# Kernel tuning notes

Measured on AMD Instinct MI355X. Metric: run time of the kernel, lower is better.

Reference implementation:

```python
import jax, jax.numpy as jnp
import numpy as np

BETA = 0.25
EPS = 1e-10


def setup_inputs() -> dict:
    key = jax.random.key(0)
    k1, k2 = jax.random.split(key)
    z = jax.random.normal(k1, (16, 256, 32, 32), dtype=jnp.float32)
    # Original init: uniform(-1/n_embed, 1/n_embed)
    n_embed, embed_dim = 8192, 256
    codebook = jax.random.uniform(k2, (n_embed, embed_dim), dtype=jnp.float32,
                                  minval=-1.0 / n_embed, maxval=1.0 / n_embed)
    return {"z": z, "codebook": codebook}


def reference(z, codebook):
    B, C, H, W = z.shape
    n_embed = codebook.shape[0]
    zp = jnp.transpose(z, (0, 2, 3, 1))            # (B,H,W,C)
    zf = zp.reshape(-1, C)                          # (N,C)
    # squared L2 distances (N, n_embed)
    d = (jnp.sum(zf * zf, axis=1, keepdims=True)
         + jnp.sum(codebook * codebook, axis=1)
         - 2.0 * zf @ codebook.T)
    idx = jnp.argmin(d, axis=1)                     # (N,)
    zq = codebook[idx].reshape(zp.shape)            # gather == one-hot @ codebook
    commitment_loss = jnp.mean((jax.lax.stop_gradient(zq) - zp) ** 2)
    embedding_loss = jnp.mean((zq - jax.lax.stop_gradient(zp)) ** 2)
    loss = embedding_loss + BETA * commitment_loss
    # straight-through estimator
    zq_st = zp + jax.lax.stop_gradient(zq - zp)
    # perplexity from mean one-hot usage (counts / N)
    counts = jnp.zeros((n_embed,), dtype=zf.dtype).at[idx].add(1.0)
    avg_probs = counts / zf.shape[0]
    perplexity = jnp.exp(-jnp.sum(avg_probs * jnp.log(avg_probs + EPS)))
    zq_out = jnp.transpose(zq_st, (0, 3, 1, 2))     # (B,C,H,W)
    return zq_out, loss, perplexity, idx
```

## Files before the change

kernel.cpp:

```cpp
#include <hip/hip_runtime.h>
#include <math.h>

#define Nrows 16384
#define NE 8192
#define Kdim 256
#define HWsz 1024
#define NSPL 4
#define BETAF 0.25f

typedef __attribute__((ext_vector_type(8))) short bf16x8;
typedef __attribute__((ext_vector_type(16))) float f32x16;
typedef unsigned short u16;

__device__ inline u16 bf16_rne(float x) {
  unsigned int u = __float_as_uint(x);
  return (u16)((u + 0x7FFFu + ((u >> 16) & 1u)) >> 16);
}
__device__ inline float bf16_tof(u16 h) {
  return __uint_as_float(((unsigned int)h) << 16);
}
__device__ inline void gll16(const void* g, void* l) {
  __builtin_amdgcn_global_load_lds(
      (const __attribute__((address_space(1))) unsigned int*)g,
      (__attribute__((address_space(3))) unsigned int*)l, 16, 0, 0);
}

__global__ __launch_bounds__(256) void cc_kernel(const float* __restrict__ cb,
                                                 float* __restrict__ cc) {
  int wave = threadIdx.x >> 6;
  int lane = threadIdx.x & 63;
  int row = blockIdx.x * 4 + wave;
  const float4 v = *(const float4*)(cb + (size_t)row * Kdim + lane * 4);
  float s = v.x * v.x + v.y * v.y + v.z * v.z + v.w * v.w;
  for (int off = 32; off; off >>= 1) s += __shfl_down(s, off);
  if (lane == 0) cc[row] = s;
}

__global__ __launch_bounds__(256) void conv_cb(const float* __restrict__ cb,
                                               u16* __restrict__ Cf) {
  const int g = blockIdx.x * 256 + threadIdx.x;
  const int j = g >> 4, k16 = g & 15;
  const float* src = cb + (size_t)j * Kdim + k16 * 16;
  float f[16];
#pragma unroll
  for (int q = 0; q < 4; ++q) {
    const float4 v = ((const float4*)src)[q];
    f[q * 4 + 0] = v.x; f[q * 4 + 1] = v.y; f[q * 4 + 2] = v.z; f[q * 4 + 3] = v.w;
  }
  u16 h[3][16];
#pragma unroll
  for (int i = 0; i < 16; ++i) {
    const u16 q0 = bf16_rne(f[i]);
    const float r1 = f[i] - bf16_tof(q0);
    const u16 q1 = bf16_rne(r1);
    const float r2 = r1 - bf16_tof(q1);
    h[0][i] = q0; h[1][i] = q1; h[2][i] = bf16_rne(r2);
  }
  const int j32 = j >> 5, li = j & 31;
#pragma unroll
  for (int arr = 0; arr < 3; ++arr) {
#pragma unroll
    for (int kh = 0; kh < 2; ++kh) {
      const size_t off = ((size_t)(j32 * 3 + arr) * 16 + k16) * 512 + (kh * 32 + li) * 8;
      *(int4*)(Cf + off) = *(int4*)&h[arr][kh * 8];
    }
  }
}

__global__ __launch_bounds__(256) void conv_z(const float* __restrict__ z,
                                              u16* __restrict__ Zf,
                                              float* __restrict__ zz) {
  __shared__ float tile[64][68];
  const int t = threadIdx.x;
  const int bid = blockIdx.x;
  const int n0 = bid * 64;
  const int b = bid >> 4;
  const int hw0 = (bid & 15) << 6;
  const float* zb = z + (size_t)b * (Kdim * HWsz) + hw0;
  float zzacc = 0.f;
  const int rr = t >> 2;
  const int kq = (t & 3) * 16;
  for (int kc = 0; kc < 4; ++kc) {
#pragma unroll
    for (int i = 0; i < 16; ++i) {
      const int idx = i * 256 + t;
      const int k = idx >> 6, r = idx & 63;
      tile[r][k] = zb[(size_t)(kc * 64 + k) * HWsz + r];
    }
    __syncthreads();
    if (t < 64) {
      for (int k = 0; k < 64; ++k) {
        const float a = tile[t][k];
        zzacc = fmaf(a, a, zzacc);
      }
    }
    u16 h[3][16];
#pragma unroll
    for (int i = 0; i < 16; ++i) {
      const float fv = tile[rr][kq + i];
      const u16 q0 = bf16_rne(fv);
      const float r1 = fv - bf16_tof(q0);
      const u16 q1 = bf16_rne(r1);
      const float r2 = r1 - bf16_tof(q1);
      h[0][i] = q0; h[1][i] = q1; h[2][i] = bf16_rne(r2);
    }
    const int k16 = kc * 4 + (t & 3);
    const int n32 = bid * 2 + (rr >> 5), li = rr & 31;
#pragma unroll
    for (int arr = 0; arr < 3; ++arr) {
#pragma unroll
      for (int kh = 0; kh < 2; ++kh) {
        const size_t off = ((size_t)(n32 * 3 + arr) * 16 + k16) * 512 + (kh * 32 + li) * 8;
        *(int4*)(Zf + off) = *(int4*)&h[arr][kh * 8];
      }
    }
    __syncthreads();
  }
  if (t < 64) zz[n0 + t] = zzacc;
}

__global__ __launch_bounds__(256, 2) void vq_gemm(
    const u16* __restrict__ Cf, const u16* __restrict__ Zf,
    const float* __restrict__ cc, const float* __restrict__ zz,
    float* __restrict__ pd, int* __restrict__ pj) {
  __shared__ __align__(16) u16 Al[2][12288];
  __shared__ float ccs[2048];

  const int t = threadIdx.x;
  const int lane = t & 63;
  const int w = __builtin_amdgcn_readfirstlane(t >> 6);
  const int bid = blockIdx.x;
  const int cg = bid & 3;
  const int rt = bid >> 2;
  const int n32 = rt * 4 + w;

#pragma unroll
  for (int i = 0; i < 8; ++i) ccs[i * 256 + t] = cc[cg * 2048 + i * 256 + t];

  const float zzv = zz[n32 * 32 + (lane & 31)];

  bf16x8 B[16][3];
#pragma unroll
  for (int kc = 0; kc < 16; ++kc)
#pragma unroll
    for (int arr = 0; arr < 3; ++arr)
      B[kc][arr] = *(const bf16x8*)(
          Zf + ((size_t)(n32 * 3 + arr) * 16 + kc) * 512 + lane * 8);

#define STAGE(gg, c_, sl)                                                     \
  if ((gg) < 32) {                                                            \
    _Pragma("unroll")                                                         \
    for (int i = 0; i < 6; ++i) {                                             \
      const int s = w * 6 + i;                                                \
      const int jx = s / 12, rem = s % 12;                                    \
      const int kc2 = rem / 3, arr = rem % 3;                                 \
      gll16(Cf + ((size_t)((cg * 64 + (gg) * 2 + jx) * 3 + arr) * 16 +        \
                  ((c_) * 4 + kc2)) * 512 + lane * 8,                         \
            &Al[sl][((jx * 4 + kc2) * 3 + arr) * 512]);                       \
    }                                                                         \
  }

#define MF(af, bv, ac) ac = __builtin_amdgcn_mfma_f32_32x32x16_bf16(af, bv, ac, 0, 0, 0);
#define CHUNK(sl, c_)                                                         \
  _Pragma("unroll")                                                           \
  for (int kc2 = 0; kc2 < 4; ++kc2) {                                         \
    bf16x8 a0[3], a1[3];                                                      \
    _Pragma("unroll")                                                         \
    for (int arr = 0; arr < 3; ++arr) {                                       \
      a0[arr] = *(const bf16x8*)&Al[sl][(kc2 * 3 + arr) * 512 + lane * 8];    \
      a1[arr] = *(const bf16x8*)&Al[sl][((4 + kc2) * 3 + arr) * 512 + lane * 8]; \
    }                                                                         \
    MF(a0[0], B[(c_) * 4 + kc2][0], acc0) MF(a1[0], B[(c_) * 4 + kc2][0], acc1) \
    MF(a0[0], B[(c_) * 4 + kc2][1], acc0) MF(a1[0], B[(c_) * 4 + kc2][1], acc1) \
    MF(a0[1], B[(c_) * 4 + kc2][0], acc0) MF(a1[1], B[(c_) * 4 + kc2][0], acc1) \
    MF(a0[1], B[(c_) * 4 + kc2][1], acc0) MF(a1[1], B[(c_) * 4 + kc2][1], acc1) \
    MF(a0[0], B[(c_) * 4 + kc2][2], acc0) MF(a1[0], B[(c_) * 4 + kc2][2], acc1) \
    MF(a0[2], B[(c_) * 4 + kc2][0], acc0) MF(a1[2], B[(c_) * 4 + kc2][0], acc1) \
  }

  STAGE(0, 0, 0)
  __syncthreads();

  float bd = INFINITY;
  int bj = 0;
  const f32x16 zero16 = {0,0,0,0,0,0,0,0,0,0,0,0,0,0,0,0};

  for (int g = 0; g < 32; ++g) {
    f32x16 acc0 = zero16, acc1 = zero16;
    STAGE(g, 1, 1)      CHUNK(0, 0) __syncthreads();
    STAGE(g, 2, 0)      CHUNK(1, 1) __syncthreads();
    STAGE(g, 3, 1)      CHUNK(0, 2) __syncthreads();
    STAGE(g + 1, 0, 0)  CHUNK(1, 3) __syncthreads();

#pragma unroll
    for (int jx = 0; jx < 2; ++jx) {
      const f32x16& a = jx ? acc1 : acc0;
#pragma unroll
      for (int q = 0; q < 4; ++q) {
        const float4 c4 = *(const float4*)&ccs[g * 64 + jx * 32 + q * 8 + (lane >> 5) * 4];
        const float cv[4] = {c4.x, c4.y, c4.z, c4.w};
#pragma unroll
        for (int r = 0; r < 4; ++r) {
          const float d = (zzv + cv[r]) - 2.0f * a[q * 4 + r];
          const int j = cg * 2048 + g * 64 + jx * 32 + r + q * 8 + (lane >> 5) * 4;
          if (d < bd) { bd = d; bj = j; }
        }
      }
    }
  }
#undef STAGE
#undef CHUNK
#undef MF

  {
    const float od = __shfl_xor(bd, 32);
    const int oj = __shfl_xor(bj, 32);
    if (od < bd || (od == bd && oj < bj)) { bd = od; bj = oj; }
  }
  if (lane < 32) {
    const int n = n32 * 32 + lane;
    pd[(size_t)cg * Nrows + n] = bd;
    pj[(size_t)cg * Nrows + n] = bj;
  }
}

__global__ __launch_bounds__(256) void vq_combine(const float* __restrict__ pd,
                                                  const int* __restrict__ pj,
                                                  int* __restrict__ idx_int,
                                                  float* __restrict__ out_idxf,
                                                  int* __restrict__ counts) {
  const int n = blockIdx.x * 256 + threadIdx.x;
  float d0 = pd[n];
  int j0 = pj[n];
  for (int s = 1; s < NSPL; ++s) {
    const float d = pd[(size_t)s * Nrows + n];
    const int j = pj[(size_t)s * Nrows + n];
    if (d < d0 || (d == d0 && j < j0)) { d0 = d; j0 = j; }
  }
  idx_int[n] = j0;
  out_idxf[n] = (float)j0;
  atomicAdd(&counts[j0], 1);
}

__global__ __launch_bounds__(256) void vq_gather_loss(
    const float* __restrict__ z, const float* __restrict__ cb,
    const int* __restrict__ idx_int, float* __restrict__ outz,
    float* __restrict__ loss_sum) {
  const int g = blockIdx.x * 256 + threadIdx.x;
  const int hw4 = g & 255;
  const int c = (g >> 8) & 255;
  const int b = g >> 16;
  const int n = b * HWsz + hw4 * 4;
  const float4 zv = *(const float4*)(z + (size_t)g * 4);
  const int4 j4 = *(const int4*)(idx_int + n);
  float4 q;
  q.x = cb[(size_t)j4.x * Kdim + c];
  q.y = cb[(size_t)j4.y * Kdim + c];
  q.z = cb[(size_t)j4.z * Kdim + c];
  q.w = cb[(size_t)j4.w * Kdim + c];
  *(float4*)(outz + (size_t)g * 4) = q;
  float dx = q.x - zv.x, dy = q.y - zv.y, dz = q.z - zv.z, dw = q.w - zv.w;
  float s = dx * dx + dy * dy + dz * dz + dw * dw;
  for (int off = 32; off; off >>= 1) s += __shfl_down(s, off);
  __shared__ float ws4[4];
  if ((threadIdx.x & 63) == 0) ws4[threadIdx.x >> 6] = s;
  __syncthreads();
  if (threadIdx.x == 0) atomicAdd(loss_sum, (ws4[0] + ws4[1]) + (ws4[2] + ws4[3]));
}

__global__ __launch_bounds__(256) void vq_final(const int* __restrict__ counts,
                                                const float* __restrict__ loss_sum,
                                                float* __restrict__ out_sc) {
  float h = 0.f;
  for (int i = threadIdx.x; i < NE; i += 256) {
    float p = (float)counts[i] * (1.0f / 16384.0f);
    h += p * logf(p + 1e-10f);
  }
  for (int off = 32; off; off >>= 1) h += __shfl_down(h, off);
  __shared__ float hs[4];
  if ((threadIdx.x & 63) == 0) hs[threadIdx.x >> 6] = h;
  __syncthreads();
  if (threadIdx.x == 0) {
    float H = (hs[0] + hs[1]) + (hs[2] + hs[3]);
    float m = loss_sum[0] * (1.0f / 4194304.0f);
    out_sc[0] = m + BETAF * m;
    out_sc[1] = expf(-H);
  }
}

extern "C" void kernel_launch(void* const* d_in, const int* in_sizes, int n_in,
                              void* d_out, int out_size, void* d_ws, size_t ws_size,
                              hipStream_t stream) {
  const float* z = (const float*)d_in[0];
  const float* cb = (const float*)d_in[1];
  float* out = (float*)d_out;
  float* out_zq = out;
  float* out_sc = out + 4194304;
  float* out_idx = out + 4194306;

  char* wp = (char*)d_ws;
  u16* Cf = (u16*)wp;           wp += (size_t)NE * Kdim * 2 * 3;
  u16* Zf = (u16*)wp;           wp += (size_t)Nrows * Kdim * 2 * 3;
  float* cc = (float*)wp;       wp += (size_t)NE * 4;
  float* zz = (float*)wp;       wp += (size_t)Nrows * 4;
  float* pd = (float*)wp;       wp += (size_t)NSPL * Nrows * 4;
  int* pj = (int*)wp;           wp += (size_t)NSPL * Nrows * 4;
  int* idx_int = (int*)wp;      wp += (size_t)Nrows * 4;
  int* counts = (int*)wp;       wp += (size_t)NE * 4;
  float* loss_sum = (float*)wp; wp += 64;

  hipMemsetAsync(counts, 0, (size_t)NE * 4, stream);
  hipMemsetAsync(loss_sum, 0, 4, stream);

  cc_kernel<<<NE / 4, 256, 0, stream>>>(cb, cc);
  conv_cb<<<NE * 16 / 256, 256, 0, stream>>>(cb, Cf);
  conv_z<<<Nrows / 64, 256, 0, stream>>>(z, Zf, zz);
  vq_gemm<<<512, 256, 0, stream>>>(Cf, Zf, cc, zz, pd, pj);
  vq_combine<<<Nrows / 256, 256, 0, stream>>>(pd, pj, idx_int, out_idx, counts);
  vq_gather_loss<<<4096, 256, 0, stream>>>(z, cb, idx_int, out_zq, loss_sum);
  vq_final<<<1, 256, 0, stream>>>(counts, loss_sum, out_sc);
}
```

Before: 480.4 us.

## Replace double-buffered codebook staging with 4-slot ring and 3-deep prefetch

Splits each codebook K-chunk into eight smaller phases staged into a 4-slot LDS ring. Loads are prefetched three phases ahead, and each phase waits only with vmcnt(6) plus a single barrier, instead of a full __syncthreads after every large chunk. MFMA sections are wrapped in s_setprio to favour the matrix issue. The aim is to hide global-to-LDS latency and cut barrier stalls. In exchange, the prefetch has no bound guard, so the last iterations load past the current codebook tile and may read out of range for the last column group.

```diff
diff --git a/kernel.cpp b/kernel.cpp
--- a/kernel.cpp
+++ b/kernel.cpp
@@ -123,7 +123,7 @@
     const u16* __restrict__ Cf, const u16* __restrict__ Zf,
     const float* __restrict__ cc, const float* __restrict__ zz,
     float* __restrict__ pd, int* __restrict__ pj) {
-  __shared__ __align__(16) u16 Al[2][12288];
+  __shared__ __align__(16) u16 Al[4][6144];
   __shared__ float ccs[2048];
 
   const int t = threadIdx.x;
@@ -147,39 +147,24 @@
       B[kc][arr] = *(const bf16x8*)(
           Zf + ((size_t)(n32 * 3 + arr) * 16 + kc) * 512 + lane * 8);
 
-#define STAGE(gg, c_, sl)                                                     \
-  if ((gg) < 32) {                                                            \
+#define STAGE(P)                                                              \
+  {                                                                           \
+    const int gg_ = (P) >> 3, ph_ = (P) & 7;                                  \
     _Pragma("unroll")                                                         \
-    for (int i = 0; i < 6; ++i) {                                             \
-      const int s = w * 6 + i;                                                \
-      const int jx = s / 12, rem = s % 12;                                    \
+    for (int i = 0; i < 3; ++i) {                                             \
+      const int s = w * 3 + i;                                                \
+      const int jx = s / 6, rem = s % 6;                                      \
       const int kc2 = rem / 3, arr = rem % 3;                                 \
-      gll16(Cf + ((size_t)((cg * 64 + (gg) * 2 + jx) * 3 + arr) * 16 +        \
-                  ((c_) * 4 + kc2)) * 512 + lane * 8,                         \
-            &Al[sl][((jx * 4 + kc2) * 3 + arr) * 512]);                       \
+      gll16(Cf + ((size_t)((cg * 64 + gg_ * 2 + jx) * 3 + arr) * 16 +         \
+                  (ph_ * 2 + kc2)) * 512 + lane * 8,                          \
+            &Al[(P) & 3][((jx * 2 + kc2) * 3 + arr) * 512]);                  \
     }                                                                         \
   }
 
 #define MF(af, bv, ac) ac = __builtin_amdgcn_mfma_f32_32x32x16_bf16(af, bv, ac, 0, 0, 0);
-#define CHUNK(sl, c_)                                                         \
-  _Pragma("unroll")                                                           \
-  for (int kc2 = 0; kc2 < 4; ++kc2) {                                         \
-    bf16x8 a0[3], a1[3];                                                      \
-    _Pragma("unroll")                                                         \
-    for (int arr = 0; arr < 3; ++arr) {                                       \
-      a0[arr] = *(const bf16x8*)&Al[sl][(kc2 * 3 + arr) * 512 + lane * 8];    \
-      a1[arr] = *(const bf16x8*)&Al[sl][((4 + kc2) * 3 + arr) * 512 + lane * 8]; \
-    }                                                                         \
-    MF(a0[0], B[(c_) * 4 + kc2][0], acc0) MF(a1[0], B[(c_) * 4 + kc2][0], acc1) \
-    MF(a0[0], B[(c_) * 4 + kc2][1], acc0) MF(a1[0], B[(c_) * 4 + kc2][1], acc1) \
-    MF(a0[1], B[(c_) * 4 + kc2][0], acc0) MF(a1[1], B[(c_) * 4 + kc2][0], acc1) \
-    MF(a0[1], B[(c_) * 4 + kc2][1], acc0) MF(a1[1], B[(c_) * 4 + kc2][1], acc1) \
-    MF(a0[0], B[(c_) * 4 + kc2][2], acc0) MF(a1[0], B[(c_) * 4 + kc2][2], acc1) \
-    MF(a0[2], B[(c_) * 4 + kc2][0], acc0) MF(a1[2], B[(c_) * 4 + kc2][0], acc1) \
-  }
-
-  STAGE(0, 0, 0)
-  __syncthreads();
+
+  STAGE(0) STAGE(1) STAGE(2)
+  asm volatile("s_waitcnt lgkmcnt(0)" ::: "memory");
 
   float bd = INFINITY;
   int bj = 0;
@@ -187,10 +172,32 @@
 
   for (int g = 0; g < 32; ++g) {
     f32x16 acc0 = zero16, acc1 = zero16;
-    STAGE(g, 1, 1)      CHUNK(0, 0) __syncthreads();
-    STAGE(g, 2, 0)      CHUNK(1, 1) __syncthreads();
-    STAGE(g, 3, 1)      CHUNK(0, 2) __syncthreads();
-    STAGE(g + 1, 0, 0)  CHUNK(1, 3) __syncthreads();
+#pragma unroll
+    for (int ph = 0; ph < 8; ++ph) {
+      __builtin_amdgcn_sched_barrier(0);
+      asm volatile("s_waitcnt vmcnt(6)" ::: "memory");
+      __builtin_amdgcn_s_barrier();
+      __builtin_amdgcn_sched_barrier(0);
+      STAGE(g * 8 + ph + 3)
+      const u16* Ab = &Al[ph & 3][0];
+      __builtin_amdgcn_s_setprio(1);
+#pragma unroll
+      for (int kc2 = 0; kc2 < 2; ++kc2) {
+        bf16x8 a0[3], a1[3];
+#pragma unroll
+        for (int arr = 0; arr < 3; ++arr) {
+          a0[arr] = *(const bf16x8*)(Ab + (kc2 * 3 + arr) * 512 + lane * 8);
+          a1[arr] = *(const bf16x8*)(Ab + ((2 + kc2) * 3 + arr) * 512 + lane * 8);
+        }
+        MF(a0[0], B[ph * 2 + kc2][0], acc0) MF(a1[0], B[ph * 2 + kc2][0], acc1)
+        MF(a0[0], B[ph * 2 + kc2][1], acc0) MF(a1[0], B[ph * 2 + kc2][1], acc1)
+        MF(a0[1], B[ph * 2 + kc2][0], acc0) MF(a1[1], B[ph * 2 + kc2][0], acc1)
+        MF(a0[1], B[ph * 2 + kc2][1], acc0) MF(a1[1], B[ph * 2 + kc2][1], acc1)
+        MF(a0[0], B[ph * 2 + kc2][2], acc0) MF(a1[0], B[ph * 2 + kc2][2], acc1)
+        MF(a0[2], B[ph * 2 + kc2][0], acc0) MF(a1[2], B[ph * 2 + kc2][0], acc1)
+      }
+      __builtin_amdgcn_s_setprio(0);
+    }
 
 #pragma unroll
     for (int jx = 0; jx < 2; ++jx) {
@@ -208,8 +215,8 @@
       }
     }
   }
+  asm volatile("s_waitcnt vmcnt(0)" ::: "memory");
 #undef STAGE
-#undef CHUNK
 #undef MF
 
   {
```

Result: slower. 517.4 us (+7.7%).
